# Optimization experiments

Measured on AMD Instinct MI355X. Metric: run time of the kernel, lower is better.

Reference implementation:

```python
import jax, jax.numpy as jnp
import numpy as np

B, H, L, D = 2, 16, 2048, 128


def setup_inputs() -> dict:
    key = jax.random.key(0)
    kq, kk, kv = jax.random.split(key, 3)
    q = jax.random.normal(kq, (B, H, L, D), dtype=jnp.float32)
    k = jax.random.normal(kk, (B, H, L, D), dtype=jnp.float32)
    v = jax.random.normal(kv, (B, H, L, D), dtype=jnp.float32)
    return {"q": q, "k": k, "v": v}


def reference(q, k, v):
    # Causal prefill attention (flash_attn_varlen_func / SDPA is_causal=True path).
    # q, k, v: [B, H, L, D]; scale = 1/sqrt(D) as in the fallback and constructor.
    Lq = q.shape[2]
    Dh = q.shape[3]
    scale = 1.0 / jnp.sqrt(jnp.asarray(Dh, q.dtype))
    scores = jnp.einsum('bhqd,bhkd->bhqk', q, k) * scale  # [B,H,Lq,Lk]
    causal = jnp.tril(jnp.ones((Lq, Lq), dtype=bool))      # [Lq,Lk]
    scores = jnp.where(causal, scores, jnp.finfo(q.dtype).min)
    probs = jax.nn.softmax(scores, axis=-1)
    return jnp.einsum('bhqk,bhkd->bhqd', probs, v)          # [B,H,Lq,D]
```

## Files before the change

### kernel.cpp

```cpp
#include <hip/hip_runtime.h>
#include <hip/hip_bf16.h>
#include <stdint.h>


#define BB 2
#define HH 16
#define LL 2048
#define DD 128

typedef float f32x4 __attribute__((ext_vector_type(4)));
typedef __bf16 bf16x8 __attribute__((ext_vector_type(8)));
typedef __bf16 bf16x2t __attribute__((ext_vector_type(2)));

union Frag16 {
    uint4    u;
    bf16x8   b;
    uint16_t s[8];
    uint32_t w32[4];
};

__device__ inline uint32_t pk2bf(float x, float y) {
    bf16x2t v;
    v.x = (__bf16)x;
    v.y = (__bf16)y;
    return __builtin_bit_cast(uint32_t, v);
}

__device__ inline uint16_t f2bf(float x) {
    uint32_t u = __builtin_bit_cast(uint32_t, x);
    u += 0x7fffu + ((u >> 16) & 1u);
    return (uint16_t)(u >> 16);
}

__device__ inline float fast_exp2(float x) {
#if __has_builtin(__builtin_amdgcn_exp2f)
    return __builtin_amdgcn_exp2f(x);
#else
    return exp2f(x);
#endif
}

__device__ __forceinline__ void stage16(const uint4* g, uint4* l) {
    __builtin_amdgcn_global_load_lds(
        (const __attribute__((address_space(1))) unsigned int*)g,
        (__attribute__((address_space(3))) unsigned int*)l, 16, 0, 0);
}

__constant__ uint8_t QT[32] = {
    31, 16,  1, 14,   18, 29, 12,  3,    4, 11, 26, 21,    9,  6, 23, 24,
     0, 15, 30, 17,   13,  2, 19, 28,   27, 20,  5, 10,   22, 25,  8,  7};

__global__ __launch_bounds__(256) void conv_kv(
    const float* __restrict__ Kg, const float* __restrict__ Vg,
    uint4* __restrict__ Kf, uint4* __restrict__ Vf)
{
    __shared__ uint16_t T[128 * 40];
    const int bid = blockIdx.x;
    const int t   = threadIdx.x;
    if (bid < 2048) {
        const int unit = bid;
        #pragma unroll
        for (int i = 0; i < 2; ++i) {
            const int local = t + i * 256;
            const int tile  = unit * 2 + (local >> 8);
            const int c     = local & 255;
            const int ds = c >> 6, quad = (c >> 4) & 3, n16 = c & 15;
            const float* p = Kg + ((size_t)tile * 16 + n16) * DD + ds * 32 + quad * 8;
            float4 a = *(const float4*)p;
            float4 b = *(const float4*)(p + 4);
            Frag16 f;
            f.w32[0] = pk2bf(a.x, a.y); f.w32[1] = pk2bf(a.z, a.w);
            f.w32[2] = pk2bf(b.x, b.y); f.w32[3] = pk2bf(b.z, b.w);
            Kf[(size_t)tile * 256 + c] = f.u;
        }
    } else {
        const int g = bid - 2048;
        const float* Vsrc = Vg + (size_t)g * 32 * DD;
        const int colg = t & 15;
        const int rp   = t >> 4;
        const int row  = rp * 2;
        const int c0   = colg * 8;
        const float* r0 = Vsrc + (size_t)row * DD + c0;
        float4 a0 = *(const float4*)(r0);
        float4 a1 = *(const float4*)(r0 + 4);
        float4 b0 = *(const float4*)(r0 + DD);
        float4 b1 = *(const float4*)(r0 + DD + 4);
        const int swz = (((row >> 3) ^ ((c0 >> 4) & 3)) << 3) + (row & 7);
        const float pa[8] = {a0.x, a0.y, a0.z, a0.w, a1.x, a1.y, a1.z, a1.w};
        const float pb[8] = {b0.x, b0.y, b0.z, b0.w, b1.x, b1.y, b1.z, b1.w};
        #pragma unroll
        for (int m = 0; m < 8; ++m)
            *(uint32_t*)&T[(c0 + m) * 40 + swz] = pk2bf(pa[m], pb[m]);
        __syncthreads();
        #pragma unroll
        for (int e2 = 0; e2 < 2; ++e2) {
            const int e   = t + e2 * 256;
            const int dt  = e >> 6;
            const int rem = e & 63;
            const int qd  = rem >> 4;
            const int nn  = rem & 15;
            const int col = dt * 16 + nn;
            const int sq  = (qd ^ ((col >> 4) & 3)) << 3;
            Frag16 f;
            f.u = *(const uint4*)&T[col * 40 + sq];
            Vf[(size_t)g * 512 + e] = f.u;
        }
    }
}

__global__ __launch_bounds__(256, 4) void fa_main(
    const float* __restrict__ Qg, const uint4* __restrict__ Kf,
    const uint4* __restrict__ Vf, float* __restrict__ Og)
{
    __shared__ __align__(16) uint4 Klds[2][512];
    __shared__ __align__(16) uint4 Vlds[2][512];
    __shared__ __align__(16) uint16_t Plds[4][16 * 40];

    const int tid  = threadIdx.x;
    const int lane = tid & 63;
    const int w    = tid >> 6;
    const int n16  = lane & 15;
    const int quad = lane >> 4;

    const int i     = blockIdx.x;
    const int xcd   = i & 7;
    const int j     = i >> 3;
    const int k4    = j & 3;
    const int bh_lo = (j >> 2) & 3;
    const int hi    = (j >> 4) & 1;
    const int a4    = j >> 5;
    const int qtile = QT[hi * 16 + a4 * 4 + k4];
    const int bh    = xcd * 4 + bh_lo;

    constexpr float kC   = 0.08838834764831845f * 1.4426950408889634f;
    constexpr float kOff = -16.0f * 1.4426950408889634f;

    float* Oh = Og + (size_t)bh * LL * DD;

    Frag16 onesf;
    #pragma unroll
    for (int z = 0; z < 8; ++z) onesf.s[z] = 0x3F80;

    const int q0  = qtile * 64;
    const int qw0 = q0 + w * 16;

    Frag16 qf[4];
    {
        const float* qrow = Qg + ((size_t)bh * LL + qw0 + n16) * DD;
        #pragma unroll
        for (int ds = 0; ds < 4; ++ds) {
            const int d0 = ds * 32 + quad * 8;
            float4 a = *(const float4*)(qrow + d0);
            float4 b = *(const float4*)(qrow + d0 + 4);
            qf[ds].w32[0] = pk2bf(a.x, a.y); qf[ds].w32[1] = pk2bf(a.z, a.w);
            qf[ds].w32[2] = pk2bf(b.x, b.y); qf[ds].w32[3] = pk2bf(b.z, b.w);
        }
    }

    f32x4 oacc[8];
    #pragma unroll
    for (int dt = 0; dt < 8; ++dt) oacc[dt] = (f32x4)0.0f;
    f32x4 lacc = (f32x4)0.0f;

    const int ns = 2 * qtile + 2;

    const uint4* sg = (w < 2 ? Kf + (size_t)(bh * 128) * 256
                             : Vf + (size_t)(bh * 64) * 512)
                      + (w & 1) * 256 + lane;
    uint4* ldb = (w < 2 ? &Klds[0][0] : &Vlds[0][0]) + (w & 1) * 256;

    auto STAGE = [&](int buf) {
        uint4* ld = ldb + buf * 512;
        #pragma unroll
        for (int c = 0; c < 4; ++c) stage16(sg + c * 64, ld + c * 64);
        sg += 512;
    };

    auto COMPUTE = [&](int buf, bool masked, int kv0) {
        const uint4* Kl = &Klds[buf][0] + lane;
        const uint4* Vl = &Vlds[buf][0] + lane;
        f32x4 sacc[2];
        sacc[0] = (f32x4)0.0f; sacc[1] = (f32x4)0.0f;
        #pragma unroll
        for (int kt = 0; kt < 2; ++kt) {
            Frag16 kfr[4];
            #pragma unroll
            for (int ds = 0; ds < 4; ++ds) kfr[ds].u = Kl[kt * 256 + ds * 64];
            __builtin_amdgcn_s_setprio(1);
            #pragma unroll
            for (int ds = 0; ds < 4; ++ds)
                sacc[kt] = __builtin_amdgcn_mfma_f32_16x16x32_bf16(
                    kfr[ds].b, qf[ds].b, sacc[kt], 0, 0, 0);
            __builtin_amdgcn_s_setprio(0);
        }
        if (masked) {
            const int qg_ = qw0 + n16;
            #pragma unroll
            for (int kt = 0; kt < 2; ++kt) {
                const int kvg = kv0 + kt * 16 + quad * 4;
                #pragma unroll
                for (int r = 0; r < 4; ++r)
                    if (kvg + r > qg_) sacc[kt][r] = -1e30f;
            }
        }
        uint16_t* pw = &Plds[w][n16 * 40];
        #pragma unroll
        for (int kt = 0; kt < 2; ++kt) {
            float p0 = fast_exp2(fmaf(sacc[kt][0], kC, kOff));
            float p1 = fast_exp2(fmaf(sacc[kt][1], kC, kOff));
            float p2 = fast_exp2(fmaf(sacc[kt][2], kC, kOff));
            float p3 = fast_exp2(fmaf(sacc[kt][3], kC, kOff));
            uint2 pw2;
            pw2.x = pk2bf(p0, p1);
            pw2.y = pk2bf(p2, p3);
            *(uint2*)&pw[kt * 16 + quad * 4] = pw2;
        }
        Frag16 pf;
        pf.u = *(const uint4*)&Plds[w][n16 * 40 + quad * 8];
        __builtin_amdgcn_s_setprio(1);
        lacc = __builtin_amdgcn_mfma_f32_16x16x32_bf16(pf.b, onesf.b, lacc, 0, 0, 0);
        __builtin_amdgcn_s_setprio(0);
        #pragma unroll
        for (int half = 0; half < 2; ++half) {
            Frag16 vf[4];
            #pragma unroll
            for (int dt = 0; dt < 4; ++dt)
                vf[dt].u = Vl[(half * 4 + dt) * 64];
            __builtin_amdgcn_s_setprio(1);
            #pragma unroll
            for (int dt = 0; dt < 4; ++dt)
                oacc[half * 4 + dt] = __builtin_amdgcn_mfma_f32_16x16x32_bf16(
                    pf.b, vf[dt].b, oacc[half * 4 + dt], 0, 0, 0);
            __builtin_amdgcn_s_setprio(0);
        }
    };

    STAGE(0);
    __syncthreads();

    int cur = 0;
    for (int t = 0; t < ns - 2; ++t) {
        STAGE(cur ^ 1);
        COMPUTE(cur, false, 0);
        __syncthreads();
        cur ^= 1;
    }
    {
        STAGE(cur ^ 1);
        COMPUTE(cur, true, (ns - 2) << 5);
        __syncthreads();
        cur ^= 1;
    }
    if (w >= 2) COMPUTE(cur, true, (ns - 1) << 5);

    #pragma unroll
    for (int r = 0; r < 4; ++r) {
        const float inv = 1.0f / lacc[r];
        float* orow = Oh + (size_t)(qw0 + quad * 4 + r) * DD + n16;
        #pragma unroll
        for (int dt = 0; dt < 8; ++dt)
            orow[dt * 16] = oacc[dt][r] * inv;
    }
}

__global__ __launch_bounds__(256) void fa_fallback(
    const float* __restrict__ Qg, const float* __restrict__ Kg,
    const float* __restrict__ Vg, float* __restrict__ Og)
{
    __shared__ uint4 Klds[32 * 16];
    __shared__ uint4 Vlds[128 * 4];
    __shared__ __align__(16) uint16_t Plds[4][32 * 40];

    const int tid  = threadIdx.x;
    const int lane = tid & 63;
    const int w    = tid >> 6;
    const int n16  = lane & 15;
    const int quad = lane >> 4;

    const int bh     = blockIdx.y;
    const int q0     = (gridDim.x - 1 - blockIdx.x) * 128;
    const int q_base = q0 + w * 32;

    const size_t base = (size_t)bh * LL * DD;
    const float* Qh = Qg + base;
    const float* Kh = Kg + base;
    const float* Vh = Vg + base;
    float*       Oh = Og + base;

    constexpr float kC = 0.08838834764831845f * 1.4426950408889634f;

    Frag16 qf[2][4];
    #pragma unroll
    for (int qt = 0; qt < 2; ++qt) {
        const float* qrow = Qh + (size_t)(q_base + qt * 16 + n16) * DD;
        #pragma unroll
        for (int ds = 0; ds < 4; ++ds) {
            const int d0 = ds * 32 + quad * 8;
            float4 a = *(const float4*)(qrow + d0);
            float4 b = *(const float4*)(qrow + d0 + 4);
            Frag16 f;
            f.s[0] = f2bf(a.x); f.s[1] = f2bf(a.y); f.s[2] = f2bf(a.z); f.s[3] = f2bf(a.w);
            f.s[4] = f2bf(b.x); f.s[5] = f2bf(b.y); f.s[6] = f2bf(b.z); f.s[7] = f2bf(b.w);
            qf[qt][ds] = f;
        }
    }

    f32x4 oacc[2][8];
    #pragma unroll
    for (int qt = 0; qt < 2; ++qt)
        #pragma unroll
        for (int dt = 0; dt < 8; ++dt) oacc[qt][dt] = (f32x4)0.0f;
    float mrow[2] = {-1e30f, -1e30f};
    float lrow[2] = {0.0f, 0.0f};

    const int ntiles = q0 / 32 + 4;

    for (int t = 0; t < ntiles; ++t) {
        const int kv0 = t * 32;
        __syncthreads();
        #pragma unroll
        for (int iu = 0; iu < 2; ++iu) {
            const int cid = tid + iu * 256;
            const int r = cid >> 4, c = cid & 15;
            const float* src = Kh + (size_t)(kv0 + r) * DD + c * 8;
            float4 a = *(const float4*)src;
            float4 b = *(const float4*)(src + 4);
            Frag16 f;
            f.s[0] = f2bf(a.x); f.s[1] = f2bf(a.y); f.s[2] = f2bf(a.z); f.s[3] = f2bf(a.w);
            f.s[4] = f2bf(b.x); f.s[5] = f2bf(b.y); f.s[6] = f2bf(b.z); f.s[7] = f2bf(b.w);
            Klds[r * 16 + (c ^ (r & 7))] = f.u;
        }
        #pragma unroll
        for (int iu = 0; iu < 2; ++iu) {
            const int cid = tid + iu * 256;
            const int d = cid >> 2, ch = cid & 3;
            const float* src = Vh + (size_t)(kv0 + ch * 8) * DD + d;
            Frag16 f;
            #pragma unroll
            for (int j = 0; j < 8; ++j) f.s[j] = f2bf(src[(size_t)j * DD]);
            Vlds[d * 4 + (ch ^ ((d >> 1) & 3))] = f.u;
        }
        __syncthreads();

        if (kv0 > q_base + 31) continue;

        f32x4 sacc[2][2];
        #pragma unroll
        for (int kt = 0; kt < 2; ++kt)
            #pragma unroll
            for (int qt = 0; qt < 2; ++qt) sacc[kt][qt] = (f32x4)0.0f;

        #pragma unroll
        for (int ds = 0; ds < 4; ++ds) {
            Frag16 kfr[2];
            #pragma unroll
            for (int kt = 0; kt < 2; ++kt) {
                const int r = kt * 16 + n16;
                const int c = ds * 4 + quad;
                kfr[kt].u = Klds[r * 16 + (c ^ (r & 7))];
            }
            #pragma unroll
            for (int kt = 0; kt < 2; ++kt)
                #pragma unroll
                for (int qt = 0; qt < 2; ++qt)
                    sacc[kt][qt] = __builtin_amdgcn_mfma_f32_16x16x32_bf16(
                        kfr[kt].b, qf[qt][ds].b, sacc[kt][qt], 0, 0, 0);
        }

        if (kv0 + 31 > q_base) {
            #pragma unroll
            for (int kt = 0; kt < 2; ++kt) {
                const int kvg = kv0 + kt * 16 + quad * 4;
                #pragma unroll
                for (int qt = 0; qt < 2; ++qt) {
                    const int qg_ = q_base + qt * 16 + n16;
                    #pragma unroll
                    for (int r = 0; r < 4; ++r)
                        if (kvg + r > qg_) sacc[kt][qt][r] = -1e30f;
                }
            }
        }

        #pragma unroll
        for (int qt = 0; qt < 2; ++qt) {
            float mt = sacc[0][qt][0];
            #pragma unroll
            for (int kt = 0; kt < 2; ++kt)
                #pragma unroll
                for (int r = 0; r < 4; ++r) mt = fmaxf(mt, sacc[kt][qt][r]);
            mt = fmaxf(mt, __shfl_xor(mt, 16));
            mt = fmaxf(mt, __shfl_xor(mt, 32));
            const float mnew  = fmaxf(mrow[qt], mt);
            const float alpha = exp2f((mrow[qt] - mnew) * kC);
            mrow[qt] = mnew;

            float ls = 0.0f;
            uint16_t* prow = &Plds[w][(qt * 16 + n16) * 40];
            #pragma unroll
            for (int kt = 0; kt < 2; ++kt)
                #pragma unroll
                for (int r = 0; r < 4; ++r) {
                    const float p = exp2f((sacc[kt][qt][r] - mnew) * kC);
                    ls += p;
                    prow[kt * 16 + quad * 4 + r] = f2bf(p);
                }
            ls += __shfl_xor(ls, 16);
            ls += __shfl_xor(ls, 32);
            lrow[qt] = lrow[qt] * alpha + ls;

            #pragma unroll
            for (int r = 0; r < 4; ++r) {
                const float ar = __shfl(alpha, quad * 4 + r);
                #pragma unroll
                for (int dt = 0; dt < 8; ++dt) oacc[qt][dt][r] *= ar;
            }
        }

        Frag16 pfr[2];
        #pragma unroll
        for (int qt = 0; qt < 2; ++qt)
            pfr[qt].u = *(const uint4*)&Plds[w][(qt * 16 + n16) * 40 + quad * 8];
        #pragma unroll
        for (int dt = 0; dt < 8; ++dt) {
            const int d = dt * 16 + n16;
            Frag16 vfr;
            vfr.u = Vlds[d * 4 + (quad ^ ((d >> 1) & 3))];
            #pragma unroll
            for (int qt = 0; qt < 2; ++qt)
                oacc[qt][dt] = __builtin_amdgcn_mfma_f32_16x16x32_bf16(
                    pfr[qt].b, vfr.b, oacc[qt][dt], 0, 0, 0);
        }
    }

    #pragma unroll
    for (int qt = 0; qt < 2; ++qt) {
        #pragma unroll
        for (int r = 0; r < 4; ++r) {
            const float lr  = __shfl(lrow[qt], quad * 4 + r);
            const float inv = 1.0f / lr;
            const int row = q_base + qt * 16 + quad * 4 + r;
            float* orow = Oh + (size_t)row * DD + n16;
            #pragma unroll
            for (int dt = 0; dt < 8; ++dt)
                orow[dt * 16] = oacc[qt][dt][r] * inv;
        }
    }
}

extern "C" void kernel_launch(void* const* d_in, const int* in_sizes, int n_in,
                              void* d_out, int out_size, void* d_ws, size_t ws_size,
                              hipStream_t stream) {
    const float* q = (const float*)d_in[0];
    const float* k = (const float*)d_in[1];
    const float* v = (const float*)d_in[2];
    float* o = (float*)d_out;

    const size_t TENS = (size_t)BB * HH * LL * DD * 2;
    if (ws_size >= 2 * TENS) {
        uint4* Kf = (uint4*)d_ws;
        uint4* Vf = (uint4*)((char*)d_ws + TENS);
        conv_kv<<<dim3(4096), dim3(256), 0, stream>>>(k, v, Kf, Vf);
        fa_main<<<dim3(1024), dim3(256), 0, stream>>>(q, Kf, Vf, o);
    } else {
        fa_fallback<<<dim3(16, BB * HH), dim3(256), 0, stream>>>(q, k, v, o);
    }
}
```

Baseline: 172.3 us.

## Split KV range across two wave groups per block and merge partial results via LDS

Each block now runs 512 threads: two groups of four waves, each handling half of the causal KV range for the same 64-query tile. The halves are combined through shared memory, reusing the K buffer to hold the second group's partial output and row sums, before normalising and writing. Blocks are now mapped to query tiles in descending order instead of through the lookup table. The aim is to shorten the serial KV loop per block and balance causal work, at the cost of doubled LDS use, a merge step, and possibly lower occupancy.

New measurement: 179.4 us. +4.1%, slower.

```diff
diff --git a/kernel.cpp b/kernel.cpp
--- a/kernel.cpp
+++ b/kernel.cpp
@@ -45,10 +45,6 @@
         (const __attribute__((address_space(1))) unsigned int*)g,
         (__attribute__((address_space(3))) unsigned int*)l, 16, 0, 0);
 }
-
-__constant__ uint8_t QT[32] = {
-    31, 16,  1, 14,   18, 29, 12,  3,    4, 11, 26, 21,    9,  6, 23, 24,
-     0, 15, 30, 17,   13,  2, 19, 28,   27, 20,  5, 10,   22, 25,  8,  7};
 
 __global__ __launch_bounds__(256) void conv_kv(
     const float* __restrict__ Kg, const float* __restrict__ Vg,
@@ -108,29 +104,29 @@
     }
 }
 
-__global__ __launch_bounds__(256, 4) void fa_main(
+__global__ __launch_bounds__(512, 4) void fa_main(
     const float* __restrict__ Qg, const uint4* __restrict__ Kf,
     const uint4* __restrict__ Vf, float* __restrict__ Og)
 {
-    __shared__ __align__(16) uint4 Klds[2][512];
-    __shared__ __align__(16) uint4 Vlds[2][512];
-    __shared__ __align__(16) uint16_t Plds[4][16 * 40];
+    __shared__ __align__(16) uint4 Klds[2][2][512];
+    __shared__ __align__(16) uint4 Vlds[2][2][512];
+    __shared__ __align__(16) uint16_t Plds[8][16 * 40];
+    __shared__ float Lbuf[4][16];
+    float* Obuf = (float*)Klds;
 
     const int tid  = threadIdx.x;
     const int lane = tid & 63;
     const int w    = tid >> 6;
     const int n16  = lane & 15;
     const int quad = lane >> 4;
-
-    const int i     = blockIdx.x;
-    const int xcd   = i & 7;
-    const int j     = i >> 3;
-    const int k4    = j & 3;
-    const int bh_lo = (j >> 2) & 3;
-    const int hi    = (j >> 4) & 1;
-    const int a4    = j >> 5;
-    const int qtile = QT[hi * 16 + a4 * 4 + k4];
-    const int bh    = xcd * 4 + bh_lo;
+    const int qh   = w & 3;
+    const int way  = w >> 2;
+
+    const int i   = blockIdx.x;
+    const int xcd = i & 7;
+    const int j   = i >> 3;
+    const int p   = 31 - (j >> 2);
+    const int bh  = xcd * 4 + (j & 3);
 
     constexpr float kC   = 0.08838834764831845f * 1.4426950408889634f;
     constexpr float kOff = -16.0f * 1.4426950408889634f;
@@ -141,8 +137,9 @@
     #pragma unroll
     for (int z = 0; z < 8; ++z) onesf.s[z] = 0x3F80;
 
-    const int q0  = qtile * 64;
-    const int qw0 = q0 + w * 16;
+    const int q0  = p * 64;
+    const int qw0 = q0 + qh * 16;
+    const int h   = p + 1;
 
     Frag16 qf[4];
     {
@@ -162,23 +159,22 @@
     for (int dt = 0; dt < 8; ++dt) oacc[dt] = (f32x4)0.0f;
     f32x4 lacc = (f32x4)0.0f;
 
-    const int ns = 2 * qtile + 2;
-
-    const uint4* sg = (w < 2 ? Kf + (size_t)(bh * 128) * 256
-                             : Vf + (size_t)(bh * 64) * 512)
-                      + (w & 1) * 256 + lane;
-    uint4* ldb = (w < 2 ? &Klds[0][0] : &Vlds[0][0]) + (w & 1) * 256;
+    uint4* kflat = &Klds[0][0][0];
+    uint4* vflat = &Vlds[0][0][0];
+    const uint4* sg = ((qh < 2) ? Kf : Vf) + (size_t)bh * 32768
+                      + (size_t)way * h * 512 + (qh & 1) * 256 + lane;
+    uint4* ldb = ((qh < 2) ? kflat : vflat) + way * 512 + (qh & 1) * 256;
 
     auto STAGE = [&](int buf) {
-        uint4* ld = ldb + buf * 512;
+        uint4* ld = ldb + buf * 1024;
         #pragma unroll
         for (int c = 0; c < 4; ++c) stage16(sg + c * 64, ld + c * 64);
         sg += 512;
     };
 
-    auto COMPUTE = [&](int buf, bool masked, int kv0) {
-        const uint4* Kl = &Klds[buf][0] + lane;
-        const uint4* Vl = &Vlds[buf][0] + lane;
+    auto COMPUTE = [&](int buf, int kv0, bool masked) {
+        const uint4* Kl = kflat + buf * 1024 + way * 512 + lane;
+        const uint4* Vl = vflat + buf * 1024 + way * 512 + lane;
         f32x4 sacc[2];
         sacc[0] = (f32x4)0.0f; sacc[1] = (f32x4)0.0f;
         #pragma unroll
@@ -222,15 +218,15 @@
         __builtin_amdgcn_s_setprio(0);
         #pragma unroll
         for (int half = 0; half < 2; ++half) {
-            Frag16 vf[4];
+            Frag16 vfr[4];
             #pragma unroll
             for (int dt = 0; dt < 4; ++dt)
-                vf[dt].u = Vl[(half * 4 + dt) * 64];
+                vfr[dt].u = Vl[(half * 4 + dt) * 64];
             __builtin_amdgcn_s_setprio(1);
             #pragma unroll
             for (int dt = 0; dt < 4; ++dt)
                 oacc[half * 4 + dt] = __builtin_amdgcn_mfma_f32_16x16x32_bf16(
-                    pf.b, vf[dt].b, oacc[half * 4 + dt], 0, 0, 0);
+                    pf.b, vfr[dt].b, oacc[half * 4 + dt], 0, 0, 0);
             __builtin_amdgcn_s_setprio(0);
         }
     };
@@ -239,27 +235,40 @@
     __syncthreads();
 
     int cur = 0;
-    for (int t = 0; t < ns - 2; ++t) {
-        STAGE(cur ^ 1);
-        COMPUTE(cur, false, 0);
+    for (int t = 0; t < h; ++t) {
+        if (t + 1 < h) STAGE(cur ^ 1);
+        const int kv0    = (way ? (h + t) : t) << 5;
+        const bool mask  = way ? (t >= h - 2) : (t == 0 && p == 0);
+        const bool activ = !(way && (t == h - 1) && (qh < 2));
+        if (activ) COMPUTE(cur, kv0, mask);
         __syncthreads();
         cur ^= 1;
     }
-    {
-        STAGE(cur ^ 1);
-        COMPUTE(cur, true, (ns - 2) << 5);
-        __syncthreads();
-        cur ^= 1;
-    }
-    if (w >= 2) COMPUTE(cur, true, (ns - 1) << 5);
-
-    #pragma unroll
-    for (int r = 0; r < 4; ++r) {
-        const float inv = 1.0f / lacc[r];
-        float* orow = Oh + (size_t)(qw0 + quad * 4 + r) * DD + n16;
+
+    if (way == 1) {
+        if (n16 == 0) {
+            #pragma unroll
+            for (int r = 0; r < 4; ++r)
+                Lbuf[qh][quad * 4 + r] = lacc[r];
+        }
         #pragma unroll
         for (int dt = 0; dt < 8; ++dt)
-            orow[dt * 16] = oacc[dt][r] * inv;
+            #pragma unroll
+            for (int r = 0; r < 4; ++r)
+                Obuf[(qh * 16 + quad * 4 + r) * 128 + dt * 16 + n16] = oacc[dt][r];
+    }
+    __syncthreads();
+    if (way == 0) {
+        #pragma unroll
+        for (int r = 0; r < 4; ++r) {
+            const float lt  = lacc[r] + Lbuf[qh][quad * 4 + r];
+            const float inv = 1.0f / lt;
+            const float* obr = &Obuf[(qh * 16 + quad * 4 + r) * 128 + n16];
+            float* orow = Oh + (size_t)(qw0 + quad * 4 + r) * DD + n16;
+            #pragma unroll
+            for (int dt = 0; dt < 8; ++dt)
+                orow[dt * 16] = (oacc[dt][r] + obr[dt * 16]) * inv;
+        }
     }
 }
 
@@ -400,9 +409,9 @@
             for (int kt = 0; kt < 2; ++kt)
                 #pragma unroll
                 for (int r = 0; r < 4; ++r) {
-                    const float p = exp2f((sacc[kt][qt][r] - mnew) * kC);
-                    ls += p;
-                    prow[kt * 16 + quad * 4 + r] = f2bf(p);
+                    const float pr = exp2f((sacc[kt][qt][r] - mnew) * kC);
+                    ls += pr;
+                    prow[kt * 16 + quad * 4 + r] = f2bf(pr);
                 }
             ls += __shfl_xor(ls, 16);
             ls += __shfl_xor(ls, 32);
@@ -460,7 +469,7 @@
         uint4* Kf = (uint4*)d_ws;
         uint4* Vf = (uint4*)((char*)d_ws + TENS);
         conv_kv<<<dim3(4096), dim3(256), 0, stream>>>(k, v, Kf, Vf);
-        fa_main<<<dim3(1024), dim3(256), 0, stream>>>(q, Kf, Vf, o);
+        fa_main<<<dim3(1024), dim3(512), 0, stream>>>(q, Kf, Vf, o);
     } else {
         fa_fallback<<<dim3(16, BB * HH), dim3(256), 0, stream>>>(q, k, v, o);
     }
```
